# Kernel optimization log

Measured on AMD Instinct MI355X. Metric: run time of the kernel, lower is better.

## Reference

```python
import jax, jax.numpy as jnp
import numpy as np

C = 512
CQK = C // 8   # 64
CV = C // 4    # 128

def setup_inputs() -> dict:
    key = jax.random.key(0)
    ks = jax.random.split(key, 10)
    B, H, W = 4, 64, 64
    s = 1.0 / np.sqrt(C)
    x = jax.random.normal(ks[0], (B, C, H, W), dtype=jnp.float32)
    Wq = jax.random.normal(ks[1], (CQK, C), dtype=jnp.float32) * s
    bq = jnp.zeros((CQK,), jnp.float32)
    Wk = jax.random.normal(ks[2], (CQK, C), dtype=jnp.float32) * s
    bk = jnp.zeros((CQK,), jnp.float32)
    Wv = jax.random.normal(ks[3], (CV, C), dtype=jnp.float32) * s
    bv = jnp.zeros((CV,), jnp.float32)
    Wo = jax.random.normal(ks[4], (C, CV), dtype=jnp.float32) * (1.0 / np.sqrt(CV))
    bo = jnp.zeros((C,), jnp.float32)
    gamma = jnp.ones((1,), jnp.float32) * 0.5  # nonzero so out path matters
    return {"x": x, "Wq": Wq, "bq": bq, "Wk": Wk, "bk": bk,
            "Wv": Wv, "bv": bv, "Wo": Wo, "bo": bo, "gamma": gamma}

def reference(x, Wq, bq, Wk, bk, Wv, bv, Wo, bo, gamma):
    B, C_, H, W = x.shape
    N = H * W
    xf = x.reshape(B, C_, N)                       # [B,C,N]
    # 1x1 convs == channel matmuls
    q = jnp.einsum('oc,bcn->bno', Wq, xf) + bq     # [B,N,Cqk]
    k = jnp.einsum('oc,bcn->bon', Wk, xf) + bk[None, :, None]  # [B,Cqk,N]
    v = jnp.einsum('oc,bcn->bon', Wv, xf) + bv[None, :, None]  # [B,Cv,N]
    attn = jax.nn.softmax(jnp.einsum('bno,bom->bnm', q, k), axis=-1)  # [B,N,N]
    out = jnp.einsum('bom,bnm->bon', v, attn)      # [B,Cv,N]
    out = jnp.einsum('oc,bcn->bon', Wo, out) + bo[None, :, None]  # [B,C,N]
    out = out.reshape(B, C_, H, W)
    return x + gamma * out
```

## Files before the change

### kernel.cpp

```cpp
#include <hip/hip_runtime.h>
#include <cstdint>
#include <cstddef>

#define N_SP 4096
#define C_IN 512
#define C_QK 64
#define C_V  128
#define LOG2E 1.4426950408889634f

typedef unsigned short u16;
typedef __attribute__((ext_vector_type(8))) short bf16x8;
typedef __attribute__((ext_vector_type(4))) float f32x4;
typedef __attribute__((ext_vector_type(16))) float f32x16;

__device__ __forceinline__ u16 f2bf(float f) {
    union { float f; uint32_t u; } x; x.f = f;
    const uint32_t r = x.u + 0x7fffu + ((x.u >> 16) & 1u);
    return (u16)(r >> 16);
}
__device__ __forceinline__ float bf2f(u16 b) {
    union { uint32_t u; float f; } x; x.u = ((uint32_t)b) << 16;
    return x.f;
}

__device__ __forceinline__ void* swzPtr(const void* base, int row, int colByte) {
    return (char*)base + row * 128 + (colByte ^ ((row & 7) << 4));
}

__global__ __launch_bounds__(256) void wconv_kernel(
    const float* __restrict__ Wq, const float* __restrict__ Wk,
    const float* __restrict__ Wv, const float* __restrict__ Wo,
    u16* __restrict__ Wqb, u16* __restrict__ Wkb,
    u16* __restrict__ Wvb, u16* __restrict__ Wob)
{
    const int i = (blockIdx.x << 8) + threadIdx.x;
    const float* src; u16* dst; int off;
    if (i < 8192)       { src = Wq; dst = Wqb; off = i; }
    else if (i < 16384) { src = Wk; dst = Wkb; off = i - 8192; }
    else if (i < 32768) { src = Wv; dst = Wvb; off = i - 16384; }
    else                { src = Wo; dst = Wob; off = i - 32768; }
    const float4 v = *(const float4*)(src + ((size_t)off << 2));
    ushort4 h;
    h.x = f2bf(v.x); h.y = f2bf(v.y); h.z = f2bf(v.z); h.w = f2bf(v.w);
    *(ushort4*)(dst + ((size_t)off << 2)) = h;
}

__global__ __launch_bounds__(256) void transpose_kernel(
    const float* __restrict__ x, u16* __restrict__ xb)
{
    __shared__ u16 ts[64 * 64];
    const int t = threadIdx.x;
    const int b  = blockIdx.x & 3;
    const int cc = (blockIdx.x >> 2) & 7;
    const int nc = blockIdx.x >> 5;
    const int c0 = cc << 6, n0 = nc << 6;
    const float* xs = x + ((size_t)(b * C_IN + c0) << 12) + n0;
    for (int u = t; u < 1024; u += 256) {
        const int c = u >> 4, nq = (u & 15) << 2;
        const float4 v = *(const float4*)(xs + ((size_t)c << 12) + nq);
        ushort4 h;
        h.x = f2bf(v.x); h.y = f2bf(v.y); h.z = f2bf(v.z); h.w = f2bf(v.w);
        *(ushort4*)((char*)ts + c * 128 + ((nq << 1) ^ (((c >> 3) & 7) << 4))) = h;
    }
    __syncthreads();
    for (int u = t; u < 512; u += 256) {
        const int n = u >> 3, cg = u & 7;
        u16 pk[8];
        #pragma unroll
        for (int j = 0; j < 8; ++j) {
            const int c = (cg << 3) + j;
            pk[j] = *(const u16*)((char*)ts + c * 128 + ((n << 1) ^ (cg << 4)));
        }
        *(ushort4*)(xb + ((size_t)((b << 12) + n0 + n) << 9) + c0 + (cg << 3)) =
            *(ushort4*)&pk[0];
        *(ushort4*)(xb + ((size_t)((b << 12) + n0 + n) << 9) + c0 + (cg << 3) + 4) =
            *(ushort4*)&pk[4];
    }
}

__global__ __launch_bounds__(256) void qkv_kernel(
    const u16* __restrict__ xb,
    const u16* __restrict__ Wqb, const float* __restrict__ bq,
    const u16* __restrict__ Wkb, const float* __restrict__ bk,
    const u16* __restrict__ Wvb, const float* __restrict__ bv,
    u16* __restrict__ Qb, u16* __restrict__ Kf, u16* __restrict__ Vf)
{
    __shared__ u16 wt[64 * 64];
    __shared__ u16 xt[64 * 64];
    const int t = threadIdx.x;
    const int l = t & 63, w = t >> 6;
    const int lo = l & 15, hi = l >> 4;
    const int b  = blockIdx.x & 3;
    const int ot = (blockIdx.x >> 2) & 3;
    const int n0 = (blockIdx.x >> 4) << 6;
    const u16* Wbase = (ot == 0) ? Wqb : (ot == 1) ? Wkb : (Wvb + ((ot - 2) << 6) * C_IN);
    f32x4 acc[4];
    #pragma unroll
    for (int ti = 0; ti < 4; ++ti) acc[ti] = (f32x4){0.f, 0.f, 0.f, 0.f};

    for (int cc = 0; cc < 8; ++cc) {
        const int c0 = cc << 6;
        for (int u = t; u < 512; u += 256) {
            const int i = u >> 3, cb = (u & 7) << 4;
            *(uint4*)swzPtr(wt, i, cb) =
                *(const uint4*)(Wbase + (size_t)i * C_IN + c0 + (cb >> 1));
        }
        for (int u = t; u < 512; u += 256) {
            const int i = u >> 3, cb = (u & 7) << 4;
            *(uint4*)swzPtr(xt, i, cb) =
                *(const uint4*)(xb + ((size_t)((b << 12) + n0 + i) << 9) + c0 + (cb >> 1));
        }
        __syncthreads();
        if (ot < 2) {
            const bf16x8 af0 = *(const bf16x8*)swzPtr(xt, (w << 4) + lo, hi << 4);
            const bf16x8 af1 = *(const bf16x8*)swzPtr(xt, (w << 4) + lo, 64 + (hi << 4));
            #pragma unroll
            for (int ti = 0; ti < 4; ++ti) {
                const bf16x8 bf0 = *(const bf16x8*)swzPtr(wt, (ti << 4) + lo, hi << 4);
                const bf16x8 bf1 = *(const bf16x8*)swzPtr(wt, (ti << 4) + lo, 64 + (hi << 4));
                acc[ti] = __builtin_amdgcn_mfma_f32_16x16x32_bf16(af0, bf0, acc[ti], 0, 0, 0);
                acc[ti] = __builtin_amdgcn_mfma_f32_16x16x32_bf16(af1, bf1, acc[ti], 0, 0, 0);
            }
        } else {
            const bf16x8 af0 = *(const bf16x8*)swzPtr(wt, (w << 4) + lo, hi << 4);
            const bf16x8 af1 = *(const bf16x8*)swzPtr(wt, (w << 4) + lo, 64 + (hi << 4));
            #pragma unroll
            for (int ti = 0; ti < 4; ++ti) {
                const bf16x8 bf0 = *(const bf16x8*)swzPtr(xt, (ti << 4) + lo, hi << 4);
                const bf16x8 bf1 = *(const bf16x8*)swzPtr(xt, (ti << 4) + lo, 64 + (hi << 4));
                acc[ti] = __builtin_amdgcn_mfma_f32_16x16x32_bf16(af0, bf0, acc[ti], 0, 0, 0);
                acc[ti] = __builtin_amdgcn_mfma_f32_16x16x32_bf16(af1, bf1, acc[ti], 0, 0, 0);
            }
        }
        __syncthreads();
    }
    const int kt = n0 >> 6;
    if (ot == 0) {
        #pragma unroll
        for (int ti = 0; ti < 4; ++ti) {
            const float bias = bq[(ti << 4) + lo];
            #pragma unroll
            for (int r = 0; r < 4; ++r) {
                const int nrow = (w << 4) + (hi << 2) + r;
                Qb[((size_t)((b << 12) + n0 + nrow) << 6) + (ti << 4) + lo] =
                    f2bf((acc[ti][r] + bias) * LOG2E);
            }
        }
    } else if (ot == 1) {
        #pragma unroll
        for (int ti = 0; ti < 4; ++ti) {
            const int ch = (ti << 4) + lo;
            const float bias = bk[ch];
            #pragma unroll
            for (int r = 0; r < 4; ++r) {
                const int key = (w << 4) + (hi << 2) + r;
                const int sid = (ti << 1) + (key >> 5);
                const int lpos = (((ch >> 3) & 1) << 5) + (key & 31);
                Kf[(((size_t)((b << 6) + kt) << 3) + sid) * 512 + (lpos << 3) + (ch & 7)] =
                    f2bf(acc[ti][r] + bias);
            }
        }
    } else {
        #pragma unroll
        for (int r = 0; r < 4; ++r) {
            const int cv = ((ot - 2) << 6) + (w << 4) + (hi << 2) + r;
            const float bias = bv[cv];
            #pragma unroll
            for (int ti = 0; ti < 4; ++ti) {
                const int nl = (ti << 4) + lo;
                const int sv = ((cv >> 5) << 2) + ti;
                const int lpos = (((nl >> 3) & 1) << 5) + (cv & 31);
                Vf[(((size_t)((b << 6) + kt) << 4) + sv) * 512 + (lpos << 3) + (nl & 7)] =
                    f2bf(acc[ti][r] + bias);
            }
        }
    }
}


#define KLOAD(dst, ktl)                                                        \
    {                                                                          \
        const size_t o_ = ((size_t)(((s << 4) + ((ktl) & 15)) << 3)) * 512;    \
        _Pragma("unroll")                                                      \
        for (int i_ = 0; i_ < 8; ++i_)                                         \
            dst[i_] = *(const bf16x8*)(kfb + o_ + i_ * 512);                   \
    }

#define VLOAD(dst, ktl, tjIdx)                                                 \
    {                                                                          \
        const size_t o_ = ((size_t)(((s << 4) + (ktl)) << 4) + ((tjIdx) << 2)) * 512; \
        _Pragma("unroll")                                                      \
        for (int i_ = 0; i_ < 4; ++i_)                                         \
            dst[i_] = *(const bf16x8*)(vfb + o_ + i_ * 512);                   \
    }

#define TILE(kt, kfU, kfP)                                                    \
    {                                                                         \
        bf16x8 vA[4], vB[4], vC[4];                                           \
        VLOAD(vA, kt, 0);                                                     \
        f32x16 sa0, sa1;                                                      \
        _Pragma("unroll")                                                     \
        for (int i = 0; i < 16; ++i) { sa0[i] = 0.f; sa1[i] = 0.f; }          \
        __builtin_amdgcn_s_setprio(1);                                        \
        _Pragma("unroll")                                                     \
        for (int ks = 0; ks < 4; ++ks) {                                      \
            sa0 = __builtin_amdgcn_mfma_f32_32x32x16_bf16(kfU[(ks << 1)], qf[ks], sa0, 0, 0, 0);     \
            sa1 = __builtin_amdgcn_mfma_f32_32x32x16_bf16(kfU[(ks << 1) + 1], qf[ks], sa1, 0, 0, 0); \
        }                                                                     \
        __builtin_amdgcn_s_setprio(0);                                        \
        KLOAD(kfP, (kt) + 1);                                                 \
        VLOAD(vB, kt, 1);                                                     \
        float p0[16], p1[16];                                                 \
        _Pragma("unroll")                                                     \
        for (int i = 0; i < 16; ++i) {                                        \
            p0[i] = exp2f(sa0[i]);                                            \
            p1[i] = exp2f(sa1[i]);                                            \
        }                                                                     \
        float sm8[8];                                                         \
        _Pragma("unroll")                                                     \
        for (int i = 0; i < 8; ++i) sm8[i] = (p0[i] + p0[i + 8]) + (p1[i] + p1[i + 8]); \
        _Pragma("unroll")                                                     \
        for (int i = 0; i < 4; ++i) sm8[i] += sm8[i + 4];                     \
        lsum += (sm8[0] + sm8[1]) + (sm8[2] + sm8[3]);                        \
        VLOAD(vC, kt, 2);                                                     \
        uint32_t P2[2][4][2];                                                 \
        _Pragma("unroll")                                                     \
        for (int g = 0; g < 4; ++g) {                                         \
            _Pragma("unroll")                                                 \
            for (int pr = 0; pr < 2; ++pr) {                                  \
                asm("v_cvt_pk_bf16_f32 %0, %1, %2"                            \
                    : "=v"(P2[0][g][pr]) : "v"(p0[4 * g + 2 * pr]), "v"(p0[4 * g + 2 * pr + 1])); \
                asm("v_cvt_pk_bf16_f32 %0, %1, %2"                            \
                    : "=v"(P2[1][g][pr]) : "v"(p1[4 * g + 2 * pr]), "v"(p1[4 * g + 2 * pr + 1])); \
            }                                                                 \
        }                                                                     \
        bf16x8 pf[4];                                                         \
        _Pragma("unroll")                                                     \
        for (int ks = 0; ks < 4; ++ks) {                                      \
            const int iE = ks << 1, iO = iE + 1;                              \
            uint32_t fr[4];                                                   \
            _Pragma("unroll")                                                 \
            for (int pr = 0; pr < 2; ++pr) {                                  \
                uint32_t X = P2[iE >> 2][iE & 3][pr];                         \
                uint32_t Y = P2[iO >> 2][iO & 3][pr];                         \
                asm("v_permlane32_swap_b32 %0, %1" : "+v"(X), "+v"(Y));       \
                fr[pr]     = X;                            \
                fr[2 + pr] = Y;                            \
            }                                                                 \
            pf[ks] = *(bf16x8*)fr;                                            \
        }                                                                     \
        __builtin_amdgcn_s_setprio(1);                                        \
        _Pragma("unroll")                                                     \
        for (int ks = 0; ks < 4; ++ks)                                        \
            oacc[0] = __builtin_amdgcn_mfma_f32_32x32x16_bf16(vA[ks], pf[ks], oacc[0], 0, 0, 0); \
        __builtin_amdgcn_s_setprio(0);                                        \
        VLOAD(vA, kt, 3);                                                     \
        __builtin_amdgcn_s_setprio(1);                                        \
        _Pragma("unroll")                                                     \
        for (int ks = 0; ks < 4; ++ks)                                        \
            oacc[1] = __builtin_amdgcn_mfma_f32_32x32x16_bf16(vB[ks], pf[ks], oacc[1], 0, 0, 0); \
        _Pragma("unroll")                                                     \
        for (int ks = 0; ks < 4; ++ks)                                        \
            oacc[2] = __builtin_amdgcn_mfma_f32_32x32x16_bf16(vC[ks], pf[ks], oacc[2], 0, 0, 0); \
        _Pragma("unroll")                                                     \
        for (int ks = 0; ks < 4; ++ks)                                        \
            oacc[3] = __builtin_amdgcn_mfma_f32_32x32x16_bf16(vA[ks], pf[ks], oacc[3], 0, 0, 0); \
        __builtin_amdgcn_s_setprio(0);                                        \
    }

__global__ __launch_bounds__(256, 2) void attn_kernel(
    const u16* __restrict__ Qb, const u16* __restrict__ Kf,
    const u16* __restrict__ Vf, u16* __restrict__ po,
    float* __restrict__ pl)
{
    const int t = threadIdx.x;
    const int l = t & 63, w = t >> 6;
    const int l31 = l & 31, h = l >> 5;
    const int b = blockIdx.x & 3;
    const int s = (blockIdx.x >> 2) & 3;
    const int qc = blockIdx.x >> 4;
    const int n0 = qc << 7;

    const u16* qp = Qb + ((size_t)((b << 12) + n0 + (w << 5) + l31) << 6) + (h << 3);
    bf16x8 qf[4];
    #pragma unroll
    for (int ks = 0; ks < 4; ++ks) qf[ks] = *(const bf16x8*)(qp + (ks << 4));

    const u16* kfb = Kf + (((size_t)(b << 6)) << 12) + (l << 3);
    const u16* vfb = Vf + (((size_t)(b << 6)) << 13) + (l << 3);

    float lsum = 0.f;
    f32x16 oacc[4];
    #pragma unroll
    for (int tj = 0; tj < 4; ++tj)
        #pragma unroll
        for (int i = 0; i < 16; ++i) oacc[tj][i] = 0.f;

    bf16x8 kfA[8], kfB[8];
    KLOAD(kfA, 0);

    for (int kt2 = 0; kt2 < 16; kt2 += 2) {
        TILE(kt2, kfA, kfB);
        TILE(kt2 + 1, kfB, kfA);
    }

    lsum += __shfl_xor(lsum, 32);
    u16* pod = po + ((size_t)blockIdx.x << 14);
    #pragma unroll
    for (int tj = 0; tj < 4; ++tj)
        #pragma unroll
        for (int r = 0; r < 16; ++r) {
            const int cv = (tj << 5) + (r & 3) + ((r >> 2) << 3) + (h << 2);
            pod[(cv << 7) + (w << 5) + l31] = f2bf(oacc[tj][r]);
        }
    if (h == 0) pl[(blockIdx.x << 7) + (w << 5) + l31] = lsum;
}

__global__ __launch_bounds__(256) void combine_kernel(
    const u16* __restrict__ po, const float* __restrict__ pl,
    u16* __restrict__ Ob)
{
    __shared__ float invl[128];
    __shared__ float tr[64][132];
    const int t = threadIdx.x;
    const int b = blockIdx.x & 3;
    const int qc = blockIdx.x >> 2;
    int slot[4];
    #pragma unroll
    for (int s = 0; s < 4; ++s) slot[s] = b + (s << 2) + (qc << 4);
    if (t < 128) {
        float lg = 0.f;
        #pragma unroll
        for (int s = 0; s < 4; ++s) lg += pl[(slot[s] << 7) + t];
        invl[t] = 1.0f / lg;
    }
    __syncthreads();
    #pragma unroll
    for (int qh = 0; qh < 2; ++qh) {
        for (int u = t; u < 2048; u += 256) {
            const int cv = u >> 4, q4 = (u & 15) << 2;
            const int q = (qh << 6) + q4;
            float a0 = 0.f, a1 = 0.f, a2 = 0.f, a3 = 0.f;
            #pragma unroll
            for (int s = 0; s < 4; ++s) {
                const ushort4 hv =
                    *(const ushort4*)(po + ((size_t)slot[s] << 14) + (cv << 7) + q);
                a0 += bf2f(hv.x); a1 += bf2f(hv.y);
                a2 += bf2f(hv.z); a3 += bf2f(hv.w);
            }
            tr[q4 + 0][cv] = a0 * invl[q];
            tr[q4 + 1][cv] = a1 * invl[q + 1];
            tr[q4 + 2][cv] = a2 * invl[q + 2];
            tr[q4 + 3][cv] = a3 * invl[q + 3];
        }
        __syncthreads();
        for (int u = t; u < 2048; u += 256) {
            const int q = u >> 5, c4 = (u & 31) << 2;
            const float4 v = *(const float4*)&tr[q][c4];
            ushort4 o;
            o.x = f2bf(v.x); o.y = f2bf(v.y); o.z = f2bf(v.z); o.w = f2bf(v.w);
            const int n = (qc << 7) + (qh << 6) + q;
            *(ushort4*)(Ob + ((size_t)((b << 12) + n) << 7) + c4) = o;
        }
        __syncthreads();
    }
}

__global__ __launch_bounds__(256) void proj_kernel(
    const u16* __restrict__ Ob, const u16* __restrict__ Wob,
    const float* __restrict__ bo, const float* __restrict__ x,
    const float* __restrict__ gamma_p, float* __restrict__ out)
{
    __shared__ union {
        struct { u16 wl0[64 * 64]; u16 wl1[64 * 64]; u16 ob0[64 * 64]; u16 ob1[64 * 64]; } s;
        float tr[64 * 64];
    } sm;
    const int t = threadIdx.x;
    const int l = t & 63, w = t >> 6;
    const int lo = l & 15, hi = l >> 4;
    const int b  = blockIdx.x & 3;
    const int co0 = ((blockIdx.x >> 2) & 7) << 6;
    const int n0  = (blockIdx.x >> 5) << 6;
    for (int u = t; u < 1024; u += 256) {
        const int i = u >> 4, cb = (u & 15) << 4;
        *(uint4*)swzPtr((cb < 128) ? sm.s.wl0 : sm.s.wl1, i, cb & 127) =
            *(const uint4*)(Wob + (size_t)(co0 + i) * C_V + (cb >> 1));
    }
    for (int u = t; u < 1024; u += 256) {
        const int i = u >> 4, cb = (u & 15) << 4;
        *(uint4*)swzPtr((cb < 128) ? sm.s.ob0 : sm.s.ob1, i, cb & 127) =
            *(const uint4*)(Ob + ((size_t)((b << 12) + n0 + i) << 7) + (cb >> 1));
    }
    __syncthreads();
    const int arow = (w << 4) + lo;
    const bf16x8 af00 = *(const bf16x8*)swzPtr(sm.s.wl0, arow, hi << 4);
    const bf16x8 af01 = *(const bf16x8*)swzPtr(sm.s.wl0, arow, 64 + (hi << 4));
    const bf16x8 af10 = *(const bf16x8*)swzPtr(sm.s.wl1, arow, hi << 4);
    const bf16x8 af11 = *(const bf16x8*)swzPtr(sm.s.wl1, arow, 64 + (hi << 4));
    f32x4 acc[4];
    #pragma unroll
    for (int ti = 0; ti < 4; ++ti) {
        const int brow = (ti << 4) + lo;
        f32x4 z = (f32x4){0.f, 0.f, 0.f, 0.f};
        z = __builtin_amdgcn_mfma_f32_16x16x32_bf16(af00, *(const bf16x8*)swzPtr(sm.s.ob0, brow, hi << 4), z, 0, 0, 0);
        z = __builtin_amdgcn_mfma_f32_16x16x32_bf16(af01, *(const bf16x8*)swzPtr(sm.s.ob0, brow, 64 + (hi << 4)), z, 0, 0, 0);
        z = __builtin_amdgcn_mfma_f32_16x16x32_bf16(af10, *(const bf16x8*)swzPtr(sm.s.ob1, brow, hi << 4), z, 0, 0, 0);
        acc[ti] = __builtin_amdgcn_mfma_f32_16x16x32_bf16(af11, *(const bf16x8*)swzPtr(sm.s.ob1, brow, 64 + (hi << 4)), z, 0, 0, 0);
    }
    __syncthreads();
    #pragma unroll
    for (int ti = 0; ti < 4; ++ti)
        #pragma unroll
        for (int r = 0; r < 4; ++r) {
            const int co = (w << 4) + (hi << 2) + r;
            const int n  = (ti << 4) + lo;
            sm.tr[(co << 6) + (n ^ (((co >> 2) & 3) << 2))] = acc[ti][r];
        }
    __syncthreads();
    const float g = gamma_p[0];
    for (int u = t; u < 1024; u += 256) {
        const int co = u >> 4, n4 = (u & 15) << 2;
        const float4 av = *(const float4*)&sm.tr[(co << 6) + (n4 ^ (((co >> 2) & 3) << 2))];
        const int o = co0 + co;
        const size_t off = ((size_t)(b * C_IN + o) << 12) + n0 + n4;
        const float4 xv = *(const float4*)(x + off);
        const float bias = bo[o];
        float4 rs;
        rs.x = xv.x + g * (av.x + bias);
        rs.y = xv.y + g * (av.y + bias);
        rs.z = xv.z + g * (av.z + bias);
        rs.w = xv.w + g * (av.w + bias);
        *(float4*)(out + off) = rs;
    }
}

extern "C" void kernel_launch(void* const* d_in, const int* in_sizes, int n_in,
                              void* d_out, int out_size, void* d_ws, size_t ws_size,
                              hipStream_t stream) {
    (void)in_sizes; (void)n_in; (void)out_size; (void)ws_size;
    const float* x  = (const float*)d_in[0];
    const float* Wq = (const float*)d_in[1];
    const float* bq = (const float*)d_in[2];
    const float* Wk = (const float*)d_in[3];
    const float* bk = (const float*)d_in[4];
    const float* Wv = (const float*)d_in[5];
    const float* bv = (const float*)d_in[6];
    const float* Wo = (const float*)d_in[7];
    const float* bo = (const float*)d_in[8];
    const float* gm = (const float*)d_in[9];
    float* out = (float*)d_out;
    u16* xb = (u16*)d_ws;
    u16* po = (u16*)d_ws;
    u16* Qb = (u16*)((char*)d_ws + ((size_t)16 << 20));
    u16* Kf = Qb + (size_t)4 * N_SP * C_QK;
    u16* Vf = Kf + (size_t)4 * N_SP * C_QK;
    float* pl = (float*)((char*)d_ws + ((size_t)24 << 20));
    u16* Ob = (u16*)((char*)d_ws + ((size_t)24 << 20) + (256 << 10));
    u16* Wqb = (u16*)((char*)d_ws + ((size_t)24 << 20) + (256 << 10) + ((size_t)4 << 20));
    u16* Wkb = Wqb + 64 * 512;
    u16* Wvb = Wkb + 64 * 512;
    u16* Wob = Wvb + 128 * 512;
    wconv_kernel<<<192, 256, 0, stream>>>(Wq, Wk, Wv, Wo, Wqb, Wkb, Wvb, Wob);
    transpose_kernel<<<2048, 256, 0, stream>>>(x, xb);
    qkv_kernel<<<1024, 256, 0, stream>>>(xb, Wqb, bq, Wkb, bk, Wvb, bv, Qb, Kf, Vf);
    attn_kernel<<<512, 256, 0, stream>>>(Qb, Kf, Vf, po, pl);
    combine_kernel<<<128, 256, 0, stream>>>(po, pl, Ob);
    proj_kernel<<<2048, 256, 0, stream>>>(Ob, Wob, bo, x, gm, out);
}
```

Before: 104.4 us.

## Fuse weight conversion into transpose, stagger attention key order, split combine blocks

```diff
diff --git a/kernel.cpp b/kernel.cpp
--- a/kernel.cpp
+++ b/kernel.cpp
@@ -27,29 +27,28 @@
     return (char*)base + row * 128 + (colByte ^ ((row & 7) << 4));
 }
 
-__global__ __launch_bounds__(256) void wconv_kernel(
+__global__ __launch_bounds__(256) void transpose_kernel(
+    const float* __restrict__ x, u16* __restrict__ xb,
     const float* __restrict__ Wq, const float* __restrict__ Wk,
     const float* __restrict__ Wv, const float* __restrict__ Wo,
     u16* __restrict__ Wqb, u16* __restrict__ Wkb,
     u16* __restrict__ Wvb, u16* __restrict__ Wob)
 {
-    const int i = (blockIdx.x << 8) + threadIdx.x;
-    const float* src; u16* dst; int off;
-    if (i < 8192)       { src = Wq; dst = Wqb; off = i; }
-    else if (i < 16384) { src = Wk; dst = Wkb; off = i - 8192; }
-    else if (i < 32768) { src = Wv; dst = Wvb; off = i - 16384; }
-    else                { src = Wo; dst = Wob; off = i - 32768; }
-    const float4 v = *(const float4*)(src + ((size_t)off << 2));
-    ushort4 h;
-    h.x = f2bf(v.x); h.y = f2bf(v.y); h.z = f2bf(v.z); h.w = f2bf(v.w);
-    *(ushort4*)(dst + ((size_t)off << 2)) = h;
-}
-
-__global__ __launch_bounds__(256) void transpose_kernel(
-    const float* __restrict__ x, u16* __restrict__ xb)
-{
+    const int t = threadIdx.x;
+    if (blockIdx.x >= 2048) {
+        const int i = ((blockIdx.x - 2048) << 8) + t;
+        const float* src; u16* dst; int off;
+        if (i < 8192)       { src = Wq; dst = Wqb; off = i; }
+        else if (i < 16384) { src = Wk; dst = Wkb; off = i - 8192; }
+        else if (i < 32768) { src = Wv; dst = Wvb; off = i - 16384; }
+        else                { src = Wo; dst = Wob; off = i - 32768; }
+        const float4 v = *(const float4*)(src + ((size_t)off << 2));
+        ushort4 h;
+        h.x = f2bf(v.x); h.y = f2bf(v.y); h.z = f2bf(v.z); h.w = f2bf(v.w);
+        *(ushort4*)(dst + ((size_t)off << 2)) = h;
+        return;
+    }
     __shared__ u16 ts[64 * 64];
-    const int t = threadIdx.x;
     const int b  = blockIdx.x & 3;
     const int cc = (blockIdx.x >> 2) & 7;
     const int nc = blockIdx.x >> 5;
@@ -188,7 +187,7 @@
 
 #define VLOAD(dst, ktl, tjIdx)                                                 \
     {                                                                          \
-        const size_t o_ = ((size_t)(((s << 4) + (ktl)) << 4) + ((tjIdx) << 2)) * 512; \
+        const size_t o_ = ((size_t)(((s << 4) + ((ktl) & 15)) << 4) + ((tjIdx) << 2)) * 512; \
         _Pragma("unroll")                                                      \
         for (int i_ = 0; i_ < 4; ++i_)                                         \
             dst[i_] = *(const bf16x8*)(vfb + o_ + i_ * 512);                   \
@@ -280,6 +279,7 @@
     const int s = (blockIdx.x >> 2) & 3;
     const int qc = blockIdx.x >> 4;
     const int n0 = qc << 7;
+    const int kt0 = ((blockIdx.x >> 8) & 1) << 3;
 
     const u16* qp = Qb + ((size_t)((b << 12) + n0 + (w << 5) + l31) << 6) + (h << 3);
     bf16x8 qf[4];
@@ -297,11 +297,11 @@
         for (int i = 0; i < 16; ++i) oacc[tj][i] = 0.f;
 
     bf16x8 kfA[8], kfB[8];
-    KLOAD(kfA, 0);
-
-    for (int kt2 = 0; kt2 < 16; kt2 += 2) {
-        TILE(kt2, kfA, kfB);
-        TILE(kt2 + 1, kfB, kfA);
+    KLOAD(kfA, kt0);
+
+    for (int kk = 0; kk < 16; kk += 2) {
+        TILE(kt0 + kk, kfA, kfB);
+        TILE(kt0 + kk + 1, kfB, kfA);
     }
 
     lsum += __shfl_xor(lsum, 32);
@@ -320,49 +320,47 @@
     const u16* __restrict__ po, const float* __restrict__ pl,
     u16* __restrict__ Ob)
 {
-    __shared__ float invl[128];
+    __shared__ float invl[64];
     __shared__ float tr[64][132];
     const int t = threadIdx.x;
     const int b = blockIdx.x & 3;
-    const int qc = blockIdx.x >> 2;
+    const int qh = (blockIdx.x >> 2) & 1;
+    const int qc = blockIdx.x >> 3;
     int slot[4];
     #pragma unroll
     for (int s = 0; s < 4; ++s) slot[s] = b + (s << 2) + (qc << 4);
-    if (t < 128) {
+    if (t < 64) {
+        const int q = (qh << 6) + t;
         float lg = 0.f;
         #pragma unroll
-        for (int s = 0; s < 4; ++s) lg += pl[(slot[s] << 7) + t];
+        for (int s = 0; s < 4; ++s) lg += pl[(slot[s] << 7) + q];
         invl[t] = 1.0f / lg;
     }
     __syncthreads();
-    #pragma unroll
-    for (int qh = 0; qh < 2; ++qh) {
-        for (int u = t; u < 2048; u += 256) {
-            const int cv = u >> 4, q4 = (u & 15) << 2;
-            const int q = (qh << 6) + q4;
-            float a0 = 0.f, a1 = 0.f, a2 = 0.f, a3 = 0.f;
-            #pragma unroll
-            for (int s = 0; s < 4; ++s) {
-                const ushort4 hv =
-                    *(const ushort4*)(po + ((size_t)slot[s] << 14) + (cv << 7) + q);
-                a0 += bf2f(hv.x); a1 += bf2f(hv.y);
-                a2 += bf2f(hv.z); a3 += bf2f(hv.w);
-            }
-            tr[q4 + 0][cv] = a0 * invl[q];
-            tr[q4 + 1][cv] = a1 * invl[q + 1];
-            tr[q4 + 2][cv] = a2 * invl[q + 2];
-            tr[q4 + 3][cv] = a3 * invl[q + 3];
-        }
-        __syncthreads();
-        for (int u = t; u < 2048; u += 256) {
-            const int q = u >> 5, c4 = (u & 31) << 2;
-            const float4 v = *(const float4*)&tr[q][c4];
-            ushort4 o;
-            o.x = f2bf(v.x); o.y = f2bf(v.y); o.z = f2bf(v.z); o.w = f2bf(v.w);
-            const int n = (qc << 7) + (qh << 6) + q;
-            *(ushort4*)(Ob + ((size_t)((b << 12) + n) << 7) + c4) = o;
-        }
-        __syncthreads();
+    for (int u = t; u < 2048; u += 256) {
+        const int cv = u >> 4, q4 = (u & 15) << 2;
+        const int q = (qh << 6) + q4;
+        float a0 = 0.f, a1 = 0.f, a2 = 0.f, a3 = 0.f;
+        #pragma unroll
+        for (int s = 0; s < 4; ++s) {
+            const ushort4 hv =
+                *(const ushort4*)(po + ((size_t)slot[s] << 14) + (cv << 7) + q);
+            a0 += bf2f(hv.x); a1 += bf2f(hv.y);
+            a2 += bf2f(hv.z); a3 += bf2f(hv.w);
+        }
+        tr[q4 + 0][cv] = a0 * invl[q4 + 0];
+        tr[q4 + 1][cv] = a1 * invl[q4 + 1];
+        tr[q4 + 2][cv] = a2 * invl[q4 + 2];
+        tr[q4 + 3][cv] = a3 * invl[q4 + 3];
+    }
+    __syncthreads();
+    for (int u = t; u < 2048; u += 256) {
+        const int q = u >> 5, c4 = (u & 31) << 2;
+        const float4 v = *(const float4*)&tr[q][c4];
+        ushort4 o;
+        o.x = f2bf(v.x); o.y = f2bf(v.y); o.z = f2bf(v.z); o.w = f2bf(v.w);
+        const int n = (qc << 7) + (qh << 6) + q;
+        *(ushort4*)(Ob + ((size_t)((b << 12) + n) << 7) + c4) = o;
     }
 }
 
@@ -460,10 +458,10 @@
     u16* Wkb = Wqb + 64 * 512;
     u16* Wvb = Wkb + 64 * 512;
     u16* Wob = Wvb + 128 * 512;
-    wconv_kernel<<<192, 256, 0, stream>>>(Wq, Wk, Wv, Wo, Wqb, Wkb, Wvb, Wob);
-    transpose_kernel<<<2048, 256, 0, stream>>>(x, xb);
+    transpose_kernel<<<2240, 256, 0, stream>>>(x, xb, Wq, Wk, Wv, Wo,
+                                               Wqb, Wkb, Wvb, Wob);
     qkv_kernel<<<1024, 256, 0, stream>>>(xb, Wqb, bq, Wkb, bk, Wvb, bv, Qb, Kf, Vf);
     attn_kernel<<<512, 256, 0, stream>>>(Qb, Kf, Vf, po, pl);
-    combine_kernel<<<128, 256, 0, stream>>>(po, pl, Ob);
+    combine_kernel<<<256, 256, 0, stream>>>(po, pl, Ob);
     proj_kernel<<<2048, 256, 0, stream>>>(Ob, Wob, bo, x, gm, out);
 }
```

After: 96.30 us. 1.08x faster.
